# Kernel tuning notes

Hardware: AMD Instinct MI355X
Metric: run time of the kernel (lower is better)

## Reference

```python
import jax, jax.numpy as jnp
import numpy as np

B, S, D = 2, 2048, 512
P, T, MAP_H = 13, 5, 64


def setup_inputs() -> dict:
    key = jax.random.key(0)
    ks = jax.random.split(key, 8)
    s = 0.02
    return {
        "hidden_states": jax.random.normal(ks[0], (B, S, D), jnp.float32),
        "ln_gamma": jnp.ones((D,), jnp.float32),
        "ln_beta": jnp.zeros((D,), jnp.float32),
        "W_in": jax.random.normal(ks[1], (D, P * D), jnp.float32) * s,
        "b_in": jnp.zeros((P * D,), jnp.float32),
        "W_map1": jax.random.normal(ks[2], (D, MAP_H), jnp.float32) * s,
        "b_map1": jnp.zeros((MAP_H,), jnp.float32),
        "W_map2": jax.random.normal(ks[3], (MAP_H, T), jnp.float32) * s,
        "b_map2": jnp.zeros((T,), jnp.float32),
        "log_tau": jnp.linspace(0.0, 4.0, T).astype(jnp.float32),
        "mix": jax.random.normal(ks[4], (P, T), jnp.float32) / float(P * T),
        "W_out": jax.random.normal(ks[5], (D, D), jnp.float32) * s,
        "b_out": jnp.zeros((D,), jnp.float32),
        "scale": jnp.float32(1e-3),
        "h_prev": jnp.zeros((B, P, T, D), jnp.float32),
        "position_offset": 0,
    }


def _forward(hidden_states, ln_gamma, ln_beta, W_in, b_in, W_map1, b_map1,
             W_map2, b_map2, log_tau, mix, W_out, b_out, scale, h_prev):
    b, s_len, d = hidden_states.shape
    p, t = mix.shape
    # pre-norm (LayerNorm, eps=1e-5)
    mu = jnp.mean(hidden_states, -1, keepdims=True)
    var = jnp.var(hidden_states, -1, keepdims=True)
    xn = (hidden_states - mu) * jax.lax.rsqrt(var + 1e-5) * ln_gamma + ln_beta
    # per-protofilament input drive: [B,S,P,D]
    u = (xn @ W_in + b_in).reshape(b, s_len, p, d)
    # liquid (input-dependent) decay per time scale: [B,S,T]
    gate = jax.nn.sigmoid(jnp.tanh(xn @ W_map1 + b_map1) @ W_map2 + b_map2)
    alpha = jnp.exp(-gate / jnp.exp(log_tau))  # [B,S,T]

    def step(h, inp):
        u_t, a_t = inp                      # [B,P,D], [B,T]
        a = a_t[:, None, :, None]           # broadcast over P and D
        h = a * h + (1.0 - a) * u_t[:, :, None, :]   # [B,P,T,D]
        y = jnp.einsum('bptd,pt->bd', h, mix)        # mix protofilaments/time scales
        return h, y

    _, ys = jax.lax.scan(step, h_prev,
                         (jnp.moveaxis(u, 1, 0), jnp.moveaxis(alpha, 1, 0)))
    mt_out = jnp.moveaxis(ys, 0, 1) @ W_out + b_out  # [B,S,D]
    return hidden_states + scale * mt_out


def reference(hidden_states, ln_gamma, ln_beta, W_in, b_in, W_map1, b_map1,
              W_map2, b_map2, log_tau, mix, W_out, b_out, scale, h_prev,
              position_offset):
    return _forward(hidden_states, ln_gamma, ln_beta, W_in, b_in, W_map1,
                    b_map1, W_map2, b_map2, log_tau, mix, W_out, b_out,
                    scale, h_prev)
```

## Files before the change

### kernel.cpp

```cpp
#include <hip/hip_runtime.h>
#include <hip/hip_bf16.h>
#include <stdint.h>

#define BB 2
#define SS 2048
#define DD 512
#define PP 13
#define TT 5
#define MH 64
#define MM (BB*SS)
#define NV (TT*DD)
#define KK 512
#define CHUNK 16
#define NCH (SS/CHUNK)

typedef __attribute__((ext_vector_type(4))) float f32x4;
typedef __attribute__((ext_vector_type(8))) short s8v;
typedef unsigned int u32;
typedef __attribute__((address_space(3))) u32 lds_u32_t;
typedef __attribute__((address_space(1))) const u32 glb_u32_t;

__device__ __forceinline__ float bf2f(unsigned short u){
  union { unsigned int i; float f; } c; c.i = ((unsigned int)u) << 16; return c.f;
}
__device__ __forceinline__ unsigned short f2bf(float f){
  union { float f; unsigned int i; } c; c.f = f;
  unsigned int x = c.i;
  unsigned int r = (x + 0x7fffu + ((x >> 16) & 1u)) >> 16;
  return (unsigned short)r;
}
__device__ __forceinline__ void gld16(unsigned short* l, const unsigned short* g){
  __builtin_amdgcn_global_load_lds((glb_u32_t*)g, (lds_u32_t*)l, 16, 0, 0);
}

__global__ __launch_bounds__(256) void k_prep_ln(
    const float* __restrict__ hs,
    const float* __restrict__ gamma, const float* __restrict__ beta,
    const float* __restrict__ W_in, const float* __restrict__ b_in,
    const float* __restrict__ mix,  const float* __restrict__ W_out,
    const float* __restrict__ W1,
    unsigned short* __restrict__ xn_bf,
    unsigned short* __restrict__ W_vT, float* __restrict__ b_v,
    unsigned short* __restrict__ W_outT, unsigned short* __restrict__ W1T)
{
  int blk = blockIdx.x;
  if (blk < 1024){
    int tid = threadIdx.x;
    int lane = tid & 63;
    int row = blk*4 + (tid>>6);
    const float* x = hs + (size_t)row*DD + lane*8;
    float4 v0 = *(const float4*)x;
    float4 v1 = *(const float4*)(x+4);
    float s  = v0.x+v0.y+v0.z+v0.w + v1.x+v1.y+v1.z+v1.w;
    float sq = v0.x*v0.x+v0.y*v0.y+v0.z*v0.z+v0.w*v0.w
             + v1.x*v1.x+v1.y*v1.y+v1.z*v1.z+v1.w*v1.w;
    #pragma unroll
    for (int o=32;o>0;o>>=1){ s += __shfl_xor(s,o); sq += __shfl_xor(sq,o); }
    float mu   = s  * (1.f/DD);
    float var  = sq * (1.f/DD) - mu*mu;
    float rstd = rsqrtf(var + 1e-5f);
    float4 g0 = *(const float4*)(gamma + lane*8);
    float4 g1 = *(const float4*)(gamma + lane*8 + 4);
    float4 b0 = *(const float4*)(beta  + lane*8);
    float4 b1v = *(const float4*)(beta + lane*8 + 4);
    union { unsigned short us[8]; uint4 u; } pk;
    pk.us[0] = f2bf((v0.x-mu)*rstd*g0.x + b0.x);
    pk.us[1] = f2bf((v0.y-mu)*rstd*g0.y + b0.y);
    pk.us[2] = f2bf((v0.z-mu)*rstd*g0.z + b0.z);
    pk.us[3] = f2bf((v0.w-mu)*rstd*g0.w + b0.w);
    pk.us[4] = f2bf((v1.x-mu)*rstd*g1.x + b1v.x);
    pk.us[5] = f2bf((v1.y-mu)*rstd*g1.y + b1v.y);
    pk.us[6] = f2bf((v1.z-mu)*rstd*g1.z + b1v.z);
    pk.us[7] = f2bf((v1.w-mu)*rstd*g1.w + b1v.w);
    *(uint4*)(xn_bf + (size_t)row*DD + lane*8) = pk.u;
  } else if (blk < 1152){
    int idx = (blk-1024) * 256 + threadIdx.x;
    int d  = idx & (DD-1);
    int k0 = idx >> 9;
    float mx[PP][TT];
    #pragma unroll
    for (int p=0;p<PP;++p)
      #pragma unroll
      for (int t=0;t<TT;++t) mx[p][t] = mix[p*TT+t];
    float acc[TT][8];
    #pragma unroll
    for (int t=0;t<TT;++t)
      #pragma unroll
      for (int j=0;j<8;++j) acc[t][j] = 0.f;
    #pragma unroll
    for (int j=0;j<8;++j){
      int k = k0*8 + j;
      const float* wrow = W_in + (size_t)k * (PP*DD) + d;
      #pragma unroll
      for (int p=0;p<PP;++p){
        float w = wrow[p*DD];
        #pragma unroll
        for (int t=0;t<TT;++t) acc[t][j] += mx[p][t]*w;
      }
    }
    #pragma unroll
    for (int t=0;t<TT;++t){
      union { unsigned short us[8]; uint4 u; } pk;
      #pragma unroll
      for (int j=0;j<8;++j) pk.us[j] = f2bf(acc[t][j]);
      *(uint4*)(W_vT + ((size_t)(t*DD+d))*KK + k0*8) = pk.u;
    }
    if (k0 == 0){
      #pragma unroll
      for (int t=0;t<TT;++t){
        float s = 0.f;
        #pragma unroll
        for (int p=0;p<PP;++p) s += mx[p][t]*b_in[p*DD+d];
        b_v[t*DD+d] = s;
      }
    }
  } else if (blk < 1280){
    int idx = (blk-1152)*256 + threadIdx.x;
    int n  = idx & (DD-1);
    int k0 = idx >> 9;
    union { unsigned short us[8]; uint4 u; } pk;
    #pragma unroll
    for (int j=0;j<8;++j) pk.us[j] = f2bf(W_out[(size_t)(k0*8+j)*DD + n]);
    *(uint4*)(W_outT + (size_t)n*KK + k0*8) = pk.u;
  } else {
    int idx = (blk-1280)*256 + threadIdx.x;
    int n  = idx >> 6;
    int k0 = idx & 63;
    union { unsigned short us[8]; uint4 u; } pk;
    #pragma unroll
    for (int j=0;j<8;++j) pk.us[j] = f2bf(W1[(size_t)(k0*8+j)*MH + n]);
    *(uint4*)(W1T + (size_t)n*KK + k0*8) = pk.u;
  }
}

__global__ __launch_bounds__(256) void k_gate(
    const unsigned short* __restrict__ xn,
    const unsigned short* __restrict__ W1T,
    const float* __restrict__ b1, const float* __restrict__ W2,
    const float* __restrict__ b2, const float* __restrict__ ltau,
    float* __restrict__ alpha)
{
  __shared__ unsigned short lA[2][64*32];
  __shared__ unsigned short lB[2][64*32];
  int bm = blockIdx.x;
  int tid = threadIdx.x, lane = tid & 63, w = tid >> 6;
  int lr = lane & 15, kq = lane >> 4;
  const uint8_t* gA = (const uint8_t*)(xn  + (size_t)(bm*64 + w*16 + (lane>>2))*KK) + (lane&3)*16;
  const uint8_t* gB = (const uint8_t*)(W1T + (size_t)(        w*16 + (lane>>2))*KK) + (lane&3)*16;
  f32x4 acc[4];
  #pragma unroll
  for (int ni=0;ni<4;++ni) acc[ni] = (f32x4){0.f,0.f,0.f,0.f};

  auto stage = [&](int buf, int kt){
    int off = kt*64;
    gld16(&lA[buf][(w*16)*32], (const unsigned short*)(gA + off));
    gld16(&lB[buf][(w*16)*32], (const unsigned short*)(gB + off));
  };
  auto compute = [&](int buf){
    union { uint4 u; s8v v; } af, bfr[4];
    af.u = *(const uint4*)&lA[buf][(w*16+lr)*32 + kq*8];
    #pragma unroll
    for (int ni=0;ni<4;++ni) bfr[ni].u = *(const uint4*)&lB[buf][(ni*16+lr)*32 + kq*8];
    #pragma unroll
    for (int ni=0;ni<4;++ni)
      acc[ni] = __builtin_amdgcn_mfma_f32_16x16x32_bf16(af.v, bfr[ni].v, acc[ni], 0,0,0);
  };

  stage(0, 0);
  __syncthreads();
  #pragma unroll
  for (int kt=1; kt<16; ++kt){
    stage(kt&1, kt);
    compute((kt&1)^1);
    __syncthreads();
  }
  compute(1);

  float z1[4][4];
  #pragma unroll
  for (int ni=0;ni<4;++ni){
    float bb = b1[ni*16+lr];
    #pragma unroll
    for (int r=0;r<4;++r) z1[r][ni] = tanhf(acc[ni][r] + bb);
  }
  float et[TT];
  #pragma unroll
  for (int t=0;t<TT;++t) et[t] = expf(-ltau[t]);
  float a[4][TT];
  #pragma unroll
  for (int t=0;t<TT;++t){
    float w2[4];
    #pragma unroll
    for (int ni=0;ni<4;++ni) w2[ni] = W2[(ni*16+lr)*TT + t];
    #pragma unroll
    for (int r=0;r<4;++r){
      float p = z1[r][0]*w2[0] + z1[r][1]*w2[1] + z1[r][2]*w2[2] + z1[r][3]*w2[3];
      #pragma unroll
      for (int o=8;o>0;o>>=1) p += __shfl_xor(p, o);
      float z2 = p + b2[t];
      float gate = 1.f/(1.f + expf(-z2));
      a[r][t] = expf(-gate * et[t]);
    }
  }
  if (lr < TT){
    int t = lr;
    #pragma unroll
    for (int r=0;r<4;++r){
      int row = bm*64 + w*16 + kq*4 + r;
      alpha[(size_t)row*TT + t] = a[r][t];
    }
  }
}

template<int BN, int NDIM, bool OUTEPI>
__global__ __launch_bounds__(256, 4) void k_gemm(
    const unsigned short* __restrict__ A,
    const unsigned short* __restrict__ Bt,
    const float* __restrict__ bias,
    const float* __restrict__ hidden,
    const float* __restrict__ scale_p,
    float* __restrict__ outF,
    unsigned short* __restrict__ outBf)
{
  constexpr int NI  = (BN == 128) ? 4 : 2;
  constexpr int WNT = BN / 2;
  constexpr int NLD = (BN == 128) ? 4 : 3;
  __shared__ unsigned short lA[2][128*32];
  __shared__ unsigned short lB[2][BN*32];
  int bid = blockIdx.y * gridDim.x + blockIdx.x;
  int nwg = gridDim.x * gridDim.y;
  int swz = (bid & 7) * (nwg >> 3) + (bid >> 3);
  int bn = swz % gridDim.x, bm = swz / gridDim.x;
  int tid  = threadIdx.x;
  int lane = tid & 63;
  int w    = tid >> 6;
  int wm = w >> 1, wn = w & 1;
  f32x4 acc[4][NI];
  #pragma unroll
  for (int i=0;i<4;++i)
    #pragma unroll
    for (int j=0;j<NI;++j) acc[i][j] = (f32x4){0.f,0.f,0.f,0.f};

  int srow  = lane >> 2;
  int slotS = (lane & 3) ^ (srow & 3);
  const uint8_t* gA = (const uint8_t*)(A + (size_t)(bm*128 + w*32 + srow)*KK) + slotS*16;
  const uint8_t* gB;
  if constexpr (BN == 128) gB = (const uint8_t*)(Bt + (size_t)(bn*BN + w*32 + srow)*KK) + slotS*16;
  else                     gB = (const uint8_t*)(Bt + (size_t)(bn*BN + w*16 + srow)*KK) + slotS*16;
  int lr = lane & 15, kq = lane >> 4;
  int kqs = kq ^ (lr & 3);

  auto stage = [&](int buf, int kt){
    int off = kt*64;
    gld16(&lA[buf][(w*32)*32],    (const unsigned short*)(gA + off));
    gld16(&lA[buf][(w*32+16)*32], (const unsigned short*)(gA + (size_t)16*KK*2 + off));
    if constexpr (BN == 128){
      gld16(&lB[buf][(w*32)*32],    (const unsigned short*)(gB + off));
      gld16(&lB[buf][(w*32+16)*32], (const unsigned short*)(gB + (size_t)16*KK*2 + off));
    } else {
      gld16(&lB[buf][(w*16)*32],    (const unsigned short*)(gB + off));
    }
  };
  auto compute = [&](int buf){
    union { uint4 u; s8v v; } af[4], bfr[NI];
    #pragma unroll
    for (int mi=0;mi<4;++mi) af[mi].u  = *(const uint4*)&lA[buf][(wm*64+mi*16+lr)*32 + kqs*8];
    #pragma unroll
    for (int ni=0;ni<NI;++ni) bfr[ni].u = *(const uint4*)&lB[buf][(wn*WNT+ni*16+lr)*32 + kqs*8];
    #pragma unroll
    for (int mi=0;mi<4;++mi)
      #pragma unroll
      for (int ni=0;ni<NI;++ni)
        acc[mi][ni] = __builtin_amdgcn_mfma_f32_16x16x32_bf16(af[mi].v, bfr[ni].v, acc[mi][ni], 0,0,0);
  };

  stage(0, 0);
  #pragma unroll
  for (int kt=0; kt<16; ++kt){
    if (kt < 15){
      stage((kt+1)&1, kt+1);
      if constexpr (NLD == 4) asm volatile("s_waitcnt vmcnt(4)" ::: "memory");
      else                    asm volatile("s_waitcnt vmcnt(3)" ::: "memory");
    } else {
      asm volatile("s_waitcnt vmcnt(0)" ::: "memory");
    }
    __builtin_amdgcn_sched_barrier(0);
    __builtin_amdgcn_s_barrier();
    __builtin_amdgcn_sched_barrier(0);
    compute(kt&1);
    __builtin_amdgcn_sched_barrier(0);
    __builtin_amdgcn_s_barrier();
  }

  float sc = 0.f;
  if constexpr (OUTEPI) sc = *scale_p;
  #pragma unroll
  for (int mi=0;mi<4;++mi){
    #pragma unroll
    for (int ni=0;ni<NI;++ni){
      int row = bm*128 + wm*64 + mi*16 + kq*4;
      int col = bn*BN  + wn*WNT + ni*16 + lr;
      float bs = bias[col];
      f32x4 c = acc[mi][ni];
      #pragma unroll
      for (int r=0;r<4;++r){
        float val = c[r] + bs;
        size_t off = (size_t)(row+r)*NDIM + col;
        if constexpr (OUTEPI) outF[off] = hidden[off] + sc*val;
        else                  outBf[off] = f2bf(val);
      }
    }
  }
}

__global__ __launch_bounds__(320) void k_scan_a(
    const float* __restrict__ alpha,
    const unsigned short* __restrict__ v,
    float* __restrict__ L, float* __restrict__ PA,
    unsigned short* __restrict__ yloc)
{
  int blk = blockIdx.x;
  int c = blk & (NCH-1), b = blk >> 7;
  int tid = threadIdx.x;
  int t  = tid >> 6;
  int d8 = tid & 63;
  __shared__ float sAl[CHUNK*TT];
  __shared__ unsigned short yl[TT][8][DD];
  if (tid < CHUNK*TT) sAl[tid] = alpha[(size_t)(b*SS + c*CHUNK)*TT + tid];
  __syncthreads();
  const unsigned short* vp = v + (size_t)(b*SS + c*CHUNK)*NV + t*DD + d8*8;
  float g[8];
  #pragma unroll
  for (int j=0;j<8;++j) g[j] = 0.f;
  float pa = 1.f;
  #pragma unroll
  for (int half=0; half<2; ++half){
    uint4 vv[8];
    #pragma unroll
    for (int s=0;s<8;++s) vv[s] = *(const uint4*)(vp + (size_t)(half*8+s)*NV);
    #pragma unroll
    for (int s=0;s<8;++s){
      float a = sAl[(half*8+s)*TT+t], om = 1.f - a;
      const unsigned short* pv = (const unsigned short*)&vv[s];
      union { unsigned short us[8]; uint4 u; } o;
      #pragma unroll
      for (int j=0;j<8;++j){ g[j] = a*g[j] + om*bf2f(pv[j]); o.us[j] = f2bf(g[j]); }
      *(uint4*)&yl[t][s][d8*8] = o.u;
      pa *= a;
    }
    __syncthreads();
    if (t < 4){
      #pragma unroll
      for (int ii=0; ii<2; ++ii){
        int s = t*2 + ii;
        float y[8];
        #pragma unroll
        for (int j=0;j<8;++j) y[j] = 0.f;
        #pragma unroll
        for (int tt=0;tt<TT;++tt){
          uint4 gv = *(const uint4*)&yl[tt][s][d8*8];
          const unsigned short* gp = (const unsigned short*)&gv;
          #pragma unroll
          for (int j=0;j<8;++j) y[j] += bf2f(gp[j]);
        }
        union { unsigned short us[8]; uint4 u; } o;
        #pragma unroll
        for (int j=0;j<8;++j) o.us[j] = f2bf(y[j]);
        *(uint4*)(yloc + (size_t)(b*SS + c*CHUNK + half*8 + s)*DD + d8*8) = o.u;
      }
    }
    __syncthreads();
  }
  float* Lp = L + ((size_t)(b*TT+t)*NCH + c)*DD + d8*8;
  *(float4*)Lp     = (float4){g[0],g[1],g[2],g[3]};
  *(float4*)(Lp+4) = (float4){g[4],g[5],g[6],g[7]};
  if (d8 == 0) PA[(size_t)(b*TT+t)*NCH + c] = pa;
}

__global__ __launch_bounds__(512) void k_scan_b(
    const float* __restrict__ mix,
    const float* __restrict__ h_prev,
    const float* __restrict__ PA,
    const float* __restrict__ L,
    float* __restrict__ Gc)
{
  int blk = blockIdx.x;
  int t = blk % TT, b = blk / TT;
  int d = threadIdx.x;
  __shared__ float sP[NCH];
  if (d < NCH) sP[d] = PA[(size_t)(b*TT+t)*NCH + d];
  __syncthreads();
  float carry = 0.f;
  #pragma unroll
  for (int p=0;p<PP;++p)
    carry += mix[p*TT+t] * h_prev[((size_t)(b*PP+p)*TT + t)*DD + d];
  const float* Lp = L  + (size_t)(b*TT+t)*NCH*DD + d;
  float*       gc = Gc + (size_t)(b*TT+t)*NCH*DD + d;
  float buf[8], nbuf[8];
  #pragma unroll
  for (int j=0;j<8;++j) buf[j] = Lp[(size_t)j*DD];
  for (int c0=0;c0<NCH;c0+=8){
    if (c0+8 < NCH){
      #pragma unroll
      for (int j=0;j<8;++j) nbuf[j] = Lp[(size_t)(c0+8+j)*DD];
    }
    #pragma unroll
    for (int j=0;j<8;++j){
      gc[(size_t)(c0+j)*DD] = carry;
      carry = sP[c0+j]*carry + buf[j];
    }
    #pragma unroll
    for (int j=0;j<8;++j) buf[j] = nbuf[j];
  }
}

__global__ __launch_bounds__(256) void k_scan_c(
    const float* __restrict__ alpha,
    const unsigned short* __restrict__ yloc,
    const float* __restrict__ Gc,
    unsigned short* __restrict__ ybf)
{
  int blk = blockIdx.x;
  int c = blk & (NCH-1), b = blk >> 7;
  int tid = threadIdx.x;
  int s4 = tid >> 6;
  int d8 = tid & 63;
  __shared__ float sAl[CHUNK*TT];
  if (tid < CHUNK*TT) sAl[tid] = alpha[(size_t)(b*SS + c*CHUNK)*TT + tid];
  __syncthreads();
  float ca[TT][8];
  #pragma unroll
  for (int t=0;t<TT;++t){
    const float* gp = Gc + ((size_t)(b*TT+t)*NCH + c)*DD + d8*8;
    float4 c0 = *(const float4*)gp;
    float4 c1 = *(const float4*)(gp+4);
    ca[t][0]=c0.x; ca[t][1]=c0.y; ca[t][2]=c0.z; ca[t][3]=c0.w;
    ca[t][4]=c1.x; ca[t][5]=c1.y; ca[t][6]=c1.z; ca[t][7]=c1.w;
  }
  float pr[TT];
  #pragma unroll
  for (int t=0;t<TT;++t){
    float p = 1.f;
    for (int j=0;j<s4*4;++j) p *= sAl[j*TT+t];
    pr[t] = p;
  }
  const unsigned short* yp = yloc + (size_t)(b*SS + c*CHUNK)*DD + d8*8;
  unsigned short* op = ybf + (size_t)(b*SS + c*CHUNK)*DD + d8*8;
  #pragma unroll
  for (int i=0;i<4;++i){
    int s2 = s4*4 + i;
    uint4 yv = *(const uint4*)(yp + (size_t)s2*DD);
    const unsigned short* yq = (const unsigned short*)&yv;
    float y[8];
    #pragma unroll
    for (int j=0;j<8;++j) y[j] = bf2f(yq[j]);
    #pragma unroll
    for (int t=0;t<TT;++t){
      pr[t] *= sAl[s2*TT+t];
      #pragma unroll
      for (int j=0;j<8;++j) y[j] += pr[t]*ca[t][j];
    }
    union { unsigned short us[8]; uint4 u; } o;
    #pragma unroll
    for (int j=0;j<8;++j) o.us[j] = f2bf(y[j]);
    *(uint4*)(op + (size_t)s2*DD) = o.u;
  }
}

extern "C" void kernel_launch(void* const* d_in, const int* in_sizes, int n_in,
                              void* d_out, int out_size, void* d_ws, size_t ws_size,
                              hipStream_t stream)
{
  (void)in_sizes; (void)n_in; (void)out_size; (void)ws_size;
  const float* hs     = (const float*)d_in[0];
  const float* gamma  = (const float*)d_in[1];
  const float* beta   = (const float*)d_in[2];
  const float* W_in   = (const float*)d_in[3];
  const float* b_in   = (const float*)d_in[4];
  const float* W1     = (const float*)d_in[5];
  const float* b1     = (const float*)d_in[6];
  const float* W2     = (const float*)d_in[7];
  const float* b2     = (const float*)d_in[8];
  const float* ltau   = (const float*)d_in[9];
  const float* mix    = (const float*)d_in[10];
  const float* W_out  = (const float*)d_in[11];
  const float* b_out  = (const float*)d_in[12];
  const float* scale  = (const float*)d_in[13];
  const float* h_prev = (const float*)d_in[14];
  float* out = (float*)d_out;

  uint8_t* w = (uint8_t*)d_ws;
  unsigned short* xn   = (unsigned short*)(w);
  unsigned short* WvT  = (unsigned short*)(w + 4194304);
  unsigned short* WoT  = (unsigned short*)(w + 6815744);
  float* alphaB        = (float*)(w + 7340032);
  float* b_v           = (float*)(w + 7421952);
  float* PA            = (float*)(w + 7432192);
  float* L             = (float*)(w + 7437312);
  float* Gc            = (float*)(w + 10058752);
  unsigned short* vg   = (unsigned short*)(w + 12680192);
  unsigned short* ybf  = (unsigned short*)(w + 33651712);
  unsigned short* W1T  = ybf;
  unsigned short* yloc = xn;

  hipLaunchKernelGGL(k_prep_ln, dim3(1296), dim3(256), 0, stream,
                     hs, gamma, beta, W_in, b_in, mix, W_out, W1,
                     xn, WvT, b_v, WoT, W1T);
  hipLaunchKernelGGL(k_gate, dim3(MM/64), dim3(256), 0, stream, xn, W1T, b1, W2, b2, ltau, alphaB);
  hipLaunchKernelGGL((k_gemm<128,NV,false>), dim3(NV/128, MM/128), dim3(256), 0, stream,
                     xn, WvT, b_v, nullptr, nullptr, nullptr, vg);
  hipLaunchKernelGGL(k_scan_a, dim3(BB*NCH), dim3(320), 0, stream, alphaB, vg, L, PA, yloc);
  hipLaunchKernelGGL(k_scan_b, dim3(BB*TT), dim3(512), 0, stream, mix, h_prev, PA, L, Gc);
  hipLaunchKernelGGL(k_scan_c, dim3(BB*NCH), dim3(256), 0, stream, alphaB, yloc, Gc, ybf);
  hipLaunchKernelGGL((k_gemm<64,DD,true>), dim3(DD/64, MM/128), dim3(256), 0, stream,
                     ybf, WoT, b_out, hs, scale, out, nullptr);
}
```

Measured before the change: 76.86 us.

## Fuse three scan kernels into one cooperative kernel with grid syncs

Merges the chunk-local scan, the cross-chunk carry propagation and the carry-application pass into a single cooperative launch separated by grid-wide barriers. The per-chunk local outputs now stay in LDS instead of round-tripping through global memory, and two kernel launches are removed. The carry pass now runs on only 20 of 256 blocks with 256 threads each while the rest wait at the barrier. It also depends on cooperative launch succeeding with 256 co-resident blocks.

```diff
diff --git a/kernel.cpp b/kernel.cpp
--- a/kernel.cpp
+++ b/kernel.cpp
@@ -1,6 +1,9 @@
 #include <hip/hip_runtime.h>
 #include <hip/hip_bf16.h>
+#include <hip/hip_cooperative_groups.h>
 #include <stdint.h>
+
+namespace cg = cooperative_groups;
 
 #define BB 2
 #define SS 2048
@@ -313,22 +316,28 @@
   }
 }
 
-__global__ __launch_bounds__(320) void k_scan_a(
+__global__ __launch_bounds__(320) void k_scan(
     const float* __restrict__ alpha,
-    const unsigned short* __restrict__ v,
+    const unsigned short* __restrict__ vg,
+    const float* __restrict__ mix,
+    const float* __restrict__ h_prev,
     float* __restrict__ L, float* __restrict__ PA,
-    unsigned short* __restrict__ yloc)
+    float* __restrict__ Gc, unsigned short* __restrict__ ybf)
 {
+  cg::grid_group grid = cg::this_grid();
   int blk = blockIdx.x;
   int c = blk & (NCH-1), b = blk >> 7;
   int tid = threadIdx.x;
   int t  = tid >> 6;
   int d8 = tid & 63;
   __shared__ float sAl[CHUNK*TT];
+  __shared__ float sP[NCH];
   __shared__ unsigned short yl[TT][8][DD];
+  __shared__ unsigned short ys[CHUNK][DD];
   if (tid < CHUNK*TT) sAl[tid] = alpha[(size_t)(b*SS + c*CHUNK)*TT + tid];
   __syncthreads();
-  const unsigned short* vp = v + (size_t)(b*SS + c*CHUNK)*NV + t*DD + d8*8;
+
+  const unsigned short* vp = vg + (size_t)(b*SS + c*CHUNK)*NV + t*DD + d8*8;
   float g[8];
   #pragma unroll
   for (int j=0;j<8;++j) g[j] = 0.f;
@@ -366,7 +375,7 @@
         union { unsigned short us[8]; uint4 u; } o;
         #pragma unroll
         for (int j=0;j<8;++j) o.us[j] = f2bf(y[j]);
-        *(uint4*)(yloc + (size_t)(b*SS + c*CHUNK + half*8 + s)*DD + d8*8) = o.u;
+        *(uint4*)&ys[half*8+s][d8*8] = o.u;
       }
     }
     __syncthreads();
@@ -375,95 +384,82 @@
   *(float4*)Lp     = (float4){g[0],g[1],g[2],g[3]};
   *(float4*)(Lp+4) = (float4){g[4],g[5],g[6],g[7]};
   if (d8 == 0) PA[(size_t)(b*TT+t)*NCH + c] = pa;
-}
-
-__global__ __launch_bounds__(512) void k_scan_b(
-    const float* __restrict__ mix,
-    const float* __restrict__ h_prev,
-    const float* __restrict__ PA,
-    const float* __restrict__ L,
-    float* __restrict__ Gc)
-{
-  int blk = blockIdx.x;
-  int t = blk % TT, b = blk / TT;
-  int d = threadIdx.x;
-  __shared__ float sP[NCH];
-  if (d < NCH) sP[d] = PA[(size_t)(b*TT+t)*NCH + d];
-  __syncthreads();
-  float carry = 0.f;
-  #pragma unroll
-  for (int p=0;p<PP;++p)
-    carry += mix[p*TT+t] * h_prev[((size_t)(b*PP+p)*TT + t)*DD + d];
-  const float* Lp = L  + (size_t)(b*TT+t)*NCH*DD + d;
-  float*       gc = Gc + (size_t)(b*TT+t)*NCH*DD + d;
-  float buf[8], nbuf[8];
-  #pragma unroll
-  for (int j=0;j<8;++j) buf[j] = Lp[(size_t)j*DD];
-  for (int c0=0;c0<NCH;c0+=8){
-    if (c0+8 < NCH){
-      #pragma unroll
-      for (int j=0;j<8;++j) nbuf[j] = Lp[(size_t)(c0+8+j)*DD];
-    }
-    #pragma unroll
-    for (int j=0;j<8;++j){
-      gc[(size_t)(c0+j)*DD] = carry;
-      carry = sP[c0+j]*carry + buf[j];
-    }
-    #pragma unroll
-    for (int j=0;j<8;++j) buf[j] = nbuf[j];
-  }
-}
-
-__global__ __launch_bounds__(256) void k_scan_c(
-    const float* __restrict__ alpha,
-    const unsigned short* __restrict__ yloc,
-    const float* __restrict__ Gc,
-    unsigned short* __restrict__ ybf)
-{
-  int blk = blockIdx.x;
-  int c = blk & (NCH-1), b = blk >> 7;
-  int tid = threadIdx.x;
-  int s4 = tid >> 6;
-  int d8 = tid & 63;
-  __shared__ float sAl[CHUNK*TT];
-  if (tid < CHUNK*TT) sAl[tid] = alpha[(size_t)(b*SS + c*CHUNK)*TT + tid];
-  __syncthreads();
-  float ca[TT][8];
-  #pragma unroll
-  for (int t=0;t<TT;++t){
-    const float* gp = Gc + ((size_t)(b*TT+t)*NCH + c)*DD + d8*8;
-    float4 c0 = *(const float4*)gp;
-    float4 c1 = *(const float4*)(gp+4);
-    ca[t][0]=c0.x; ca[t][1]=c0.y; ca[t][2]=c0.z; ca[t][3]=c0.w;
-    ca[t][4]=c1.x; ca[t][5]=c1.y; ca[t][6]=c1.z; ca[t][7]=c1.w;
-  }
-  float pr[TT];
-  #pragma unroll
-  for (int t=0;t<TT;++t){
-    float p = 1.f;
-    for (int j=0;j<s4*4;++j) p *= sAl[j*TT+t];
-    pr[t] = p;
-  }
-  const unsigned short* yp = yloc + (size_t)(b*SS + c*CHUNK)*DD + d8*8;
-  unsigned short* op = ybf + (size_t)(b*SS + c*CHUNK)*DD + d8*8;
-  #pragma unroll
-  for (int i=0;i<4;++i){
-    int s2 = s4*4 + i;
-    uint4 yv = *(const uint4*)(yp + (size_t)s2*DD);
-    const unsigned short* yq = (const unsigned short*)&yv;
-    float y[8];
-    #pragma unroll
-    for (int j=0;j<8;++j) y[j] = bf2f(yq[j]);
-    #pragma unroll
-    for (int t=0;t<TT;++t){
-      pr[t] *= sAl[s2*TT+t];
-      #pragma unroll
-      for (int j=0;j<8;++j) y[j] += pr[t]*ca[t][j];
-    }
-    union { unsigned short us[8]; uint4 u; } o;
-    #pragma unroll
-    for (int j=0;j<8;++j) o.us[j] = f2bf(y[j]);
-    *(uint4*)(op + (size_t)s2*DD) = o.u;
+  __threadfence();
+  grid.sync();
+
+  if (blk < 2*BB*TT){
+    int bt = blk >> 1;
+    int tb = bt % TT, b2 = bt / TT;
+    if (tid < NCH) sP[tid] = PA[(size_t)bt*NCH + tid];
+    __syncthreads();
+    if (tid < 256){
+      int d = (blk & 1)*256 + tid;
+      float carry = 0.f;
+      #pragma unroll
+      for (int p=0;p<PP;++p)
+        carry += mix[p*TT+tb] * h_prev[((size_t)(b2*PP+p)*TT + tb)*DD + d];
+      const float* Lq = L  + (size_t)bt*NCH*DD + d;
+      float*       gc = Gc + (size_t)bt*NCH*DD + d;
+      float buf[8], nbuf[8];
+      #pragma unroll
+      for (int j=0;j<8;++j) buf[j] = Lq[(size_t)j*DD];
+      for (int c0=0;c0<NCH;c0+=8){
+        if (c0+8 < NCH){
+          #pragma unroll
+          for (int j=0;j<8;++j) nbuf[j] = Lq[(size_t)(c0+8+j)*DD];
+        }
+        #pragma unroll
+        for (int j=0;j<8;++j){
+          gc[(size_t)(c0+j)*DD] = carry;
+          carry = sP[c0+j]*carry + buf[j];
+        }
+        #pragma unroll
+        for (int j=0;j<8;++j) buf[j] = nbuf[j];
+      }
+    }
+    __threadfence();
+  }
+  grid.sync();
+
+  if (tid < 256){
+    int s4 = tid >> 6;
+    int dc = tid & 63;
+    float ca[TT][8];
+    #pragma unroll
+    for (int tt=0;tt<TT;++tt){
+      const float* gp = Gc + ((size_t)(b*TT+tt)*NCH + c)*DD + dc*8;
+      float4 c0 = *(const float4*)gp;
+      float4 c1 = *(const float4*)(gp+4);
+      ca[tt][0]=c0.x; ca[tt][1]=c0.y; ca[tt][2]=c0.z; ca[tt][3]=c0.w;
+      ca[tt][4]=c1.x; ca[tt][5]=c1.y; ca[tt][6]=c1.z; ca[tt][7]=c1.w;
+    }
+    float pr[TT];
+    #pragma unroll
+    for (int tt=0;tt<TT;++tt){
+      float p = 1.f;
+      for (int j=0;j<s4*4;++j) p *= sAl[j*TT+tt];
+      pr[tt] = p;
+    }
+    unsigned short* op = ybf + (size_t)(b*SS + c*CHUNK)*DD + dc*8;
+    #pragma unroll
+    for (int i=0;i<4;++i){
+      int s2 = s4*4 + i;
+      uint4 yv = *(const uint4*)&ys[s2][dc*8];
+      const unsigned short* yq = (const unsigned short*)&yv;
+      float y[8];
+      #pragma unroll
+      for (int j=0;j<8;++j) y[j] = bf2f(yq[j]);
+      #pragma unroll
+      for (int tt=0;tt<TT;++tt){
+        pr[tt] *= sAl[s2*TT+tt];
+        #pragma unroll
+        for (int j=0;j<8;++j) y[j] += pr[tt]*ca[tt][j];
+      }
+      union { unsigned short us[8]; uint4 u; } o;
+      #pragma unroll
+      for (int j=0;j<8;++j) o.us[j] = f2bf(y[j]);
+      *(uint4*)(op + (size_t)s2*DD) = o.u;
+    }
   }
 }
 
@@ -501,7 +497,6 @@
   unsigned short* vg   = (unsigned short*)(w + 12680192);
   unsigned short* ybf  = (unsigned short*)(w + 33651712);
   unsigned short* W1T  = ybf;
-  unsigned short* yloc = xn;
 
   hipLaunchKernelGGL(k_prep_ln, dim3(1296), dim3(256), 0, stream,
                      hs, gamma, beta, W_in, b_in, mix, W_out, W1,
@@ -509,9 +504,14 @@
   hipLaunchKernelGGL(k_gate, dim3(MM/64), dim3(256), 0, stream, xn, W1T, b1, W2, b2, ltau, alphaB);
   hipLaunchKernelGGL((k_gemm<128,NV,false>), dim3(NV/128, MM/128), dim3(256), 0, stream,
                      xn, WvT, b_v, nullptr, nullptr, nullptr, vg);
-  hipLaunchKernelGGL(k_scan_a, dim3(BB*NCH), dim3(320), 0, stream, alphaB, vg, L, PA, yloc);
-  hipLaunchKernelGGL(k_scan_b, dim3(BB*TT), dim3(512), 0, stream, mix, h_prev, PA, L, Gc);
-  hipLaunchKernelGGL(k_scan_c, dim3(BB*NCH), dim3(256), 0, stream, alphaB, yloc, Gc, ybf);
+  {
+    const float* a0 = alphaB; const unsigned short* a1 = vg;
+    const float* a2 = mix; const float* a3 = h_prev;
+    float* a4 = L; float* a5 = PA; float* a6 = Gc; unsigned short* a7 = ybf;
+    void* args[] = { (void*)&a0, (void*)&a1, (void*)&a2, (void*)&a3,
+                     (void*)&a4, (void*)&a5, (void*)&a6, (void*)&a7 };
+    hipLaunchCooperativeKernel((const void*)k_scan, dim3(BB*NCH), dim3(320), args, 0, stream);
+  }
   hipLaunchKernelGGL((k_gemm<64,DD,true>), dim3(DD/64, MM/128), dim3(256), 0, stream,
                      ybf, WoT, b_out, hs, scale, out, nullptr);
 }
```

Measured after the change: 185.5 us. 2.41x slower.

## Fuse gate MLP into prep kernel, recomputing LayerNorm in registers

Applied to the files above, without the earlier changes.

Removes the separate k_gate launch by adding 64 blocks to k_prep_ln. Each block converts W1 into a swizzled LDS tile, recomputes LayerNorm for its 64 rows directly from the fp32 hidden states into MFMA fragments, and computes alpha in place. This drops one kernel launch and the dependency on xn/W1T being written first. In exchange, every block of the prep kernel now declares 64KB of LDS, which can limit occupancy for the other block types, and the 64 gate blocks each redo the W1 conversion.

```diff
diff --git a/kernel.cpp b/kernel.cpp
--- a/kernel.cpp
+++ b/kernel.cpp
@@ -38,16 +38,117 @@
     const float* __restrict__ gamma, const float* __restrict__ beta,
     const float* __restrict__ W_in, const float* __restrict__ b_in,
     const float* __restrict__ mix,  const float* __restrict__ W_out,
-    const float* __restrict__ W1,
+    const float* __restrict__ W1,   const float* __restrict__ b1,
+    const float* __restrict__ W2,   const float* __restrict__ b2,
+    const float* __restrict__ ltau,
     unsigned short* __restrict__ xn_bf,
     unsigned short* __restrict__ W_vT, float* __restrict__ b_v,
-    unsigned short* __restrict__ W_outT, unsigned short* __restrict__ W1T)
+    unsigned short* __restrict__ W_outT,
+    float* __restrict__ alpha)
 {
+  __shared__ unsigned short W1L[MH][KK];
   int blk = blockIdx.x;
-  if (blk < 1024){
+  if (blk < 64){
+    int gb = blk;
+    int tid = threadIdx.x, lane = tid & 63, w = tid >> 6;
+    int lr = lane & 15, kq = lane >> 4;
+    int row = gb*64 + w*16 + lr;
+    #pragma unroll 4
+    for (int i=0;i<128;++i){
+      int idx = i*256 + tid;
+      int n = idx & 63, k = idx >> 6;
+      int slot = (k >> 3) ^ (n & 7);
+      W1L[n][slot*8 + (k & 7)] = f2bf(W1[idx]);
+    }
+    float v[16][8];
+    float s = 0.f, sq = 0.f;
+    const float* xr = hs + (size_t)row*DD + kq*8;
+    #pragma unroll
+    for (int kt=0;kt<16;++kt){
+      float4 a0 = *(const float4*)(xr + kt*32);
+      float4 a1 = *(const float4*)(xr + kt*32 + 4);
+      v[kt][0]=a0.x; v[kt][1]=a0.y; v[kt][2]=a0.z; v[kt][3]=a0.w;
+      v[kt][4]=a1.x; v[kt][5]=a1.y; v[kt][6]=a1.z; v[kt][7]=a1.w;
+      s  += a0.x+a0.y+a0.z+a0.w + a1.x+a1.y+a1.z+a1.w;
+      sq += a0.x*a0.x+a0.y*a0.y+a0.z*a0.z+a0.w*a0.w
+          + a1.x*a1.x+a1.y*a1.y+a1.z*a1.z+a1.w*a1.w;
+    }
+    s  += __shfl_xor(s,16);  s  += __shfl_xor(s,32);
+    sq += __shfl_xor(sq,16); sq += __shfl_xor(sq,32);
+    float mu   = s  * (1.f/DD);
+    float var  = sq * (1.f/DD) - mu*mu;
+    float rstd = rsqrtf(var + 1e-5f);
+    s8v af[16];
+    #pragma unroll
+    for (int kt=0;kt<16;++kt){
+      float4 g0 = *(const float4*)(gamma + kq*8 + kt*32);
+      float4 g1 = *(const float4*)(gamma + kq*8 + kt*32 + 4);
+      float4 t0 = *(const float4*)(beta  + kq*8 + kt*32);
+      float4 t1 = *(const float4*)(beta  + kq*8 + kt*32 + 4);
+      union { unsigned short us[8]; s8v v8; } o;
+      o.us[0] = f2bf((v[kt][0]-mu)*rstd*g0.x + t0.x);
+      o.us[1] = f2bf((v[kt][1]-mu)*rstd*g0.y + t0.y);
+      o.us[2] = f2bf((v[kt][2]-mu)*rstd*g0.z + t0.z);
+      o.us[3] = f2bf((v[kt][3]-mu)*rstd*g0.w + t0.w);
+      o.us[4] = f2bf((v[kt][4]-mu)*rstd*g1.x + t1.x);
+      o.us[5] = f2bf((v[kt][5]-mu)*rstd*g1.y + t1.y);
+      o.us[6] = f2bf((v[kt][6]-mu)*rstd*g1.z + t1.z);
+      o.us[7] = f2bf((v[kt][7]-mu)*rstd*g1.w + t1.w);
+      af[kt] = o.v8;
+    }
+    __syncthreads();
+    f32x4 acc[4];
+    #pragma unroll
+    for (int ni=0;ni<4;++ni) acc[ni] = (f32x4){0.f,0.f,0.f,0.f};
+    #pragma unroll
+    for (int kt=0;kt<16;++kt){
+      #pragma unroll
+      for (int ni=0;ni<4;++ni){
+        int n = ni*16 + lr;
+        int slot = (kt*4 + kq) ^ (n & 7);
+        union { uint4 u; s8v v8; } bfr;
+        bfr.u = *(const uint4*)&W1L[n][slot*8];
+        acc[ni] = __builtin_amdgcn_mfma_f32_16x16x32_bf16(af[kt], bfr.v8, acc[ni], 0,0,0);
+      }
+    }
+    float z1[4][4];
+    #pragma unroll
+    for (int ni=0;ni<4;++ni){
+      float bb = b1[ni*16+lr];
+      #pragma unroll
+      for (int r=0;r<4;++r) z1[r][ni] = tanhf(acc[ni][r] + bb);
+    }
+    float et[TT];
+    #pragma unroll
+    for (int t=0;t<TT;++t) et[t] = expf(-ltau[t]);
+    float av[4][TT];
+    #pragma unroll
+    for (int t=0;t<TT;++t){
+      float w2v[4];
+      #pragma unroll
+      for (int ni=0;ni<4;++ni) w2v[ni] = W2[(ni*16+lr)*TT + t];
+      #pragma unroll
+      for (int r=0;r<4;++r){
+        float p = z1[r][0]*w2v[0] + z1[r][1]*w2v[1] + z1[r][2]*w2v[2] + z1[r][3]*w2v[3];
+        #pragma unroll
+        for (int o=8;o>0;o>>=1) p += __shfl_xor(p, o);
+        float z2 = p + b2[t];
+        float gate = 1.f/(1.f + expf(-z2));
+        av[r][t] = expf(-gate * et[t]);
+      }
+    }
+    if (lr < TT){
+      int t = lr;
+      #pragma unroll
+      for (int r=0;r<4;++r){
+        int orow = gb*64 + w*16 + kq*4 + r;
+        alpha[(size_t)orow*TT + t] = av[r][t];
+      }
+    }
+  } else if (blk < 1088){
     int tid = threadIdx.x;
     int lane = tid & 63;
-    int row = blk*4 + (tid>>6);
+    int row = (blk-64)*4 + (tid>>6);
     const float* x = hs + (size_t)row*DD + lane*8;
     float4 v0 = *(const float4*)x;
     float4 v1 = *(const float4*)(x+4);
@@ -73,8 +174,8 @@
     pk.us[6] = f2bf((v1.z-mu)*rstd*g1.z + b1v.z);
     pk.us[7] = f2bf((v1.w-mu)*rstd*g1.w + b1v.w);
     *(uint4*)(xn_bf + (size_t)row*DD + lane*8) = pk.u;
-  } else if (blk < 1152){
-    int idx = (blk-1024) * 256 + threadIdx.x;
+  } else if (blk < 1216){
+    int idx = (blk-1088) * 256 + threadIdx.x;
     int d  = idx & (DD-1);
     int k0 = idx >> 9;
     float mx[PP][TT];
@@ -114,101 +215,14 @@
         b_v[t*DD+d] = s;
       }
     }
-  } else if (blk < 1280){
-    int idx = (blk-1152)*256 + threadIdx.x;
+  } else {
+    int idx = (blk-1216)*256 + threadIdx.x;
     int n  = idx & (DD-1);
     int k0 = idx >> 9;
     union { unsigned short us[8]; uint4 u; } pk;
     #pragma unroll
     for (int j=0;j<8;++j) pk.us[j] = f2bf(W_out[(size_t)(k0*8+j)*DD + n]);
     *(uint4*)(W_outT + (size_t)n*KK + k0*8) = pk.u;
-  } else {
-    int idx = (blk-1280)*256 + threadIdx.x;
-    int n  = idx >> 6;
-    int k0 = idx & 63;
-    union { unsigned short us[8]; uint4 u; } pk;
-    #pragma unroll
-    for (int j=0;j<8;++j) pk.us[j] = f2bf(W1[(size_t)(k0*8+j)*MH + n]);
-    *(uint4*)(W1T + (size_t)n*KK + k0*8) = pk.u;
-  }
-}
-
-__global__ __launch_bounds__(256) void k_gate(
-    const unsigned short* __restrict__ xn,
-    const unsigned short* __restrict__ W1T,
-    const float* __restrict__ b1, const float* __restrict__ W2,
-    const float* __restrict__ b2, const float* __restrict__ ltau,
-    float* __restrict__ alpha)
-{
-  __shared__ unsigned short lA[2][64*32];
-  __shared__ unsigned short lB[2][64*32];
-  int bm = blockIdx.x;
-  int tid = threadIdx.x, lane = tid & 63, w = tid >> 6;
-  int lr = lane & 15, kq = lane >> 4;
-  const uint8_t* gA = (const uint8_t*)(xn  + (size_t)(bm*64 + w*16 + (lane>>2))*KK) + (lane&3)*16;
-  const uint8_t* gB = (const uint8_t*)(W1T + (size_t)(        w*16 + (lane>>2))*KK) + (lane&3)*16;
-  f32x4 acc[4];
-  #pragma unroll
-  for (int ni=0;ni<4;++ni) acc[ni] = (f32x4){0.f,0.f,0.f,0.f};
-
-  auto stage = [&](int buf, int kt){
-    int off = kt*64;
-    gld16(&lA[buf][(w*16)*32], (const unsigned short*)(gA + off));
-    gld16(&lB[buf][(w*16)*32], (const unsigned short*)(gB + off));
-  };
-  auto compute = [&](int buf){
-    union { uint4 u; s8v v; } af, bfr[4];
-    af.u = *(const uint4*)&lA[buf][(w*16+lr)*32 + kq*8];
-    #pragma unroll
-    for (int ni=0;ni<4;++ni) bfr[ni].u = *(const uint4*)&lB[buf][(ni*16+lr)*32 + kq*8];
-    #pragma unroll
-    for (int ni=0;ni<4;++ni)
-      acc[ni] = __builtin_amdgcn_mfma_f32_16x16x32_bf16(af.v, bfr[ni].v, acc[ni], 0,0,0);
-  };
-
-  stage(0, 0);
-  __syncthreads();
-  #pragma unroll
-  for (int kt=1; kt<16; ++kt){
-    stage(kt&1, kt);
-    compute((kt&1)^1);
-    __syncthreads();
-  }
-  compute(1);
-
-  float z1[4][4];
-  #pragma unroll
-  for (int ni=0;ni<4;++ni){
-    float bb = b1[ni*16+lr];
-    #pragma unroll
-    for (int r=0;r<4;++r) z1[r][ni] = tanhf(acc[ni][r] + bb);
-  }
-  float et[TT];
-  #pragma unroll
-  for (int t=0;t<TT;++t) et[t] = expf(-ltau[t]);
-  float a[4][TT];
-  #pragma unroll
-  for (int t=0;t<TT;++t){
-    float w2[4];
-    #pragma unroll
-    for (int ni=0;ni<4;++ni) w2[ni] = W2[(ni*16+lr)*TT + t];
-    #pragma unroll
-    for (int r=0;r<4;++r){
-      float p = z1[r][0]*w2[0] + z1[r][1]*w2[1] + z1[r][2]*w2[2] + z1[r][3]*w2[3];
-      #pragma unroll
-      for (int o=8;o>0;o>>=1) p += __shfl_xor(p, o);
-      float z2 = p + b2[t];
-      float gate = 1.f/(1.f + expf(-z2));
-      a[r][t] = expf(-gate * et[t]);
-    }
-  }
-  if (lr < TT){
-    int t = lr;
-    #pragma unroll
-    for (int r=0;r<4;++r){
-      int row = bm*64 + w*16 + kq*4 + r;
-      alpha[(size_t)row*TT + t] = a[r][t];
-    }
   }
 }
 
@@ -500,13 +514,11 @@
   float* Gc            = (float*)(w + 10058752);
   unsigned short* vg   = (unsigned short*)(w + 12680192);
   unsigned short* ybf  = (unsigned short*)(w + 33651712);
-  unsigned short* W1T  = ybf;
   unsigned short* yloc = xn;
 
-  hipLaunchKernelGGL(k_prep_ln, dim3(1296), dim3(256), 0, stream,
-                     hs, gamma, beta, W_in, b_in, mix, W_out, W1,
-                     xn, WvT, b_v, WoT, W1T);
-  hipLaunchKernelGGL(k_gate, dim3(MM/64), dim3(256), 0, stream, xn, W1T, b1, W2, b2, ltau, alphaB);
+  hipLaunchKernelGGL(k_prep_ln, dim3(1344), dim3(256), 0, stream,
+                     hs, gamma, beta, W_in, b_in, mix, W_out, W1, b1, W2, b2, ltau,
+                     xn, WvT, b_v, WoT, alphaB);
   hipLaunchKernelGGL((k_gemm<128,NV,false>), dim3(NV/128, MM/128), dim3(256), 0, stream,
                      xn, WvT, b_v, nullptr, nullptr, nullptr, vg);
   hipLaunchKernelGGL(k_scan_a, dim3(BB*NCH), dim3(320), 0, stream, alphaB, vg, L, PA, yloc);
```

New measurement: 76.86 us. Within noise of the previous version (+0.0%).
